# Kernel optimization log

Hardware: AMD Instinct MI355X
Metric: run time of the kernel (lower is better)

Reference implementation:

```python
import jax, jax.numpy as jnp
import numpy as np

B, N, C = 2, 2048, 256
L, H = 4, 4
HD = C // H  # 64, div=1 so q/k keep full head dim
EPS = 1e-5   # BatchNorm eps (eval mode, running_mean=0, running_var=1)


def setup_inputs() -> dict:
    key = jax.random.key(0)
    ks = jax.random.split(key, 20)
    w = lambda k, s: jax.random.normal(k, s, jnp.float32) * 0.05
    return {
        'x': jax.random.normal(ks[0], (B, N, C), jnp.float32),
        'in_w1': w(ks[1], (C, C)), 'in_b1': w(ks[2], (C,)),
        'in_g1': 1.0 + w(ks[3], (C,)), 'in_be1': w(ks[4], (C,)),
        'in_w2': w(ks[5], (C, C)), 'in_b2': w(ks[6], (C,)),
        'in_g2': 1.0 + w(ks[7], (C,)), 'in_be2': w(ks[8], (C,)),
        'q_w': w(ks[9], (L, H, HD, HD)), 'k_w': w(ks[10], (L, H, HD, HD)),
        'v_w': w(ks[11], (L, H, HD, HD)), 'v_b': w(ks[12], (L, H, HD)),
        't_w': w(ks[13], (L, H, HD, HD)), 't_b': w(ks[14], (L, H, HD)),
        'bn_g': 1.0 + w(ks[15], (L, H, HD)), 'bn_b': w(ks[16], (L, H, HD)),
        'proj_w': w(ks[17], (L, C, C)), 'proj_b': w(ks[18], (L, C)),
    }


def _bn(t, g, b):
    # eval-mode BatchNorm1d with running_mean=0, running_var=1
    return t * (g / jnp.sqrt(1.0 + EPS))[:, None] + b[:, None]


def _forward(x, in_w1, in_b1, in_g1, in_be1, in_w2, in_b2, in_g2, in_be2,
             q_w, k_w, v_w, v_b, t_w, t_b, bn_g, bn_b, proj_w, proj_b):
    Bq, Nq, Cq = x.shape
    h = x.transpose(0, 2, 1)  # (B, C, N)
    h = jax.nn.relu(_bn(jnp.einsum('oc,bcn->bon', in_w1, h) + in_b1[:, None], in_g1, in_be1))
    h = jax.nn.relu(_bn(jnp.einsum('oc,bcn->bon', in_w2, h) + in_b2[:, None], in_g2, in_be2))
    h = h.reshape(Bq, H, HD, Nq)  # split heads (B, H, hd, N)
    for l in range(L):
        xq = jnp.einsum('hoc,bhcn->bhno', q_w[l], h)                       # (B,H,N,hd)
        xk = jnp.einsum('hoc,bhcn->bhon', k_w[l], h)                       # (B,H,hd,N)
        xv = jnp.einsum('hoc,bhcn->bhon', v_w[l], h) + v_b[l][None, :, :, None]
        attn = jax.nn.softmax(jnp.einsum('bhno,bhom->bhnm', xq, xk), axis=-1)
        # offset-attention normalization: divide by column sums (torch dim=1)
        attn = attn / (1e-9 + attn.sum(axis=2, keepdims=True))
        xr = jnp.einsum('bhcn,bhnm->bhcm', xv, attn)                       # (B,H,hd,N)
        d = h - xr
        t = jnp.einsum('hoc,bhcn->bhon', t_w[l], d) + t_b[l][None, :, :, None]
        xr = jax.nn.relu(t * (bn_g[l] / jnp.sqrt(1.0 + EPS))[None, :, :, None]
                         + bn_b[l][None, :, :, None])
        h = h + xr
        hm = h.reshape(Bq, Cq, Nq)  # concat heads
        hm = jnp.einsum('oc,bcn->bon', proj_w[l], hm) + proj_b[l][:, None]
        h = hm.reshape(Bq, H, HD, Nq)
    return h.reshape(Bq, Cq, Nq).transpose(0, 2, 1)  # (B, N, C)


def reference(x, in_w1, in_b1, in_g1, in_be1, in_w2, in_b2, in_g2, in_be2,
              q_w, k_w, v_w, v_b, t_w, t_b, bn_g, bn_b, proj_w, proj_b):
    return _forward(x, in_w1, in_b1, in_g1, in_be1, in_w2, in_b2, in_g2, in_be2,
                    q_w, k_w, v_w, v_b, t_w, t_b, bn_g, bn_b, proj_w, proj_b)
```

## Files before the change

kernel.cpp:

```cpp
#include <hip/hip_runtime.h>
#include <math.h>

constexpr int NB = 2, NN = 2048, NC = 256, NL = 4, NH = 4, ND = 64;
constexpr float EPSV = 1e-5f;

using half8 = __attribute__((ext_vector_type(8))) _Float16;
using half4 = __attribute__((ext_vector_type(4))) _Float16;
using f32x4 = __attribute__((ext_vector_type(4))) float;

__device__ __forceinline__ f32x4 mfma16(half8 a, half8 b, f32x4 c) {
    return __builtin_amdgcn_mfma_f32_16x16x32_f16(a, b, c, 0, 0, 0);
}
__device__ __forceinline__ half8 cvt8(const float* p) {
    float4 x0 = *(const float4*)p, x1 = *(const float4*)(p + 4);
    half8 h;
    h[0]=(_Float16)x0.x; h[1]=(_Float16)x0.y; h[2]=(_Float16)x0.z; h[3]=(_Float16)x0.w;
    h[4]=(_Float16)x1.x; h[5]=(_Float16)x1.y; h[6]=(_Float16)x1.z; h[7]=(_Float16)x1.w;
    return h;
}

template<int EPI, bool INF16>
__global__ __launch_bounds__(256) void gemm_mfma(
    const float* __restrict__ Wg, const float* __restrict__ bias,
    const float* __restrict__ gam, const float* __restrict__ bet,
    const void* __restrict__ inp, _Float16* __restrict__ out16)
{
    int b = blockIdx.x, o0 = blockIdx.y * 64, n0 = blockIdx.z * 32;
    int t = threadIdx.x, w = t >> 6, li = t & 15, qd = (t >> 4) & 3;
    const float* wr = Wg + (size_t)(o0 + w * 16 + li) * NC + qd * 8;
    half8 af[8];
#pragma unroll
    for (int ks = 0; ks < 8; ++ks) af[ks] = cvt8(wr + ks * 32);
    f32x4 acc[2];
    acc[0] = {0.f, 0.f, 0.f, 0.f}; acc[1] = {0.f, 0.f, 0.f, 0.f};
#pragma unroll
    for (int ks = 0; ks < 8; ++ks) {
#pragma unroll
        for (int g = 0; g < 2; ++g) {
            int n = n0 + g * 16 + li;
            half8 bf;
            if (INF16) {
                bf = *(const half8*)((const _Float16*)inp +
                        ((size_t)(b * NN + n) * NC + ks * 32 + qd * 8));
            } else {
                bf = cvt8((const float*)inp + ((size_t)(b * NN + n) * NC + ks * 32 + qd * 8));
            }
            acc[g] = mfma16(af[ks], bf, acc[g]);
        }
    }
    int ob = o0 + w * 16 + qd * 4;
    float4 bs = *(const float4*)(bias + ob);
    float4 gs = {0,0,0,0}, be = {0,0,0,0};
    if (EPI == 1) { gs = *(const float4*)(gam + ob); be = *(const float4*)(bet + ob); }
    float scl = rsqrtf(1.f + EPSV);
#pragma unroll
    for (int g = 0; g < 2; ++g) {
        int n = n0 + g * 16 + li;
        half4 hv;
#pragma unroll
        for (int r = 0; r < 4; ++r) {
            float v = acc[g][r] + ((const float*)&bs)[r];
            if (EPI == 1)
                v = fmaxf(0.f, v * (((const float*)&gs)[r] * scl) + ((const float*)&be)[r]);
            hv[r] = (_Float16)v;
        }
        *(half4*)(out16 + (size_t)(b * NN + n) * NC + ob) = hv;
    }
}

__global__ __launch_bounds__(256) void qkv_fused(
    const float* __restrict__ qw, const float* __restrict__ kw,
    const float* __restrict__ vw, const float* __restrict__ vb,
    const _Float16* __restrict__ h16, _Float16* __restrict__ q16,
    _Float16* __restrict__ k16, _Float16* __restrict__ v16, int l)
{
    int bh = blockIdx.x, n0 = blockIdx.y * 64;
    int hh = bh & 3, b = bh >> 2;
    size_t wbase = (size_t)(l * NH + hh) * ND * ND;
    int t = threadIdx.x, w = t >> 6, li = t & 15, qd = (t >> 4) & 3;
    size_t wro = (size_t)(w * 16 + li) * ND + qd * 8;
    half8 aq0 = cvt8(qw + wbase + wro), aq1 = cvt8(qw + wbase + wro + 32);
    half8 ak0 = cvt8(kw + wbase + wro), ak1 = cvt8(kw + wbase + wro + 32);
    half8 av0 = cvt8(vw + wbase + wro), av1 = cvt8(vw + wbase + wro + 32);
    f32x4 accq[4], acck[4], accv[4];
#pragma unroll
    for (int g = 0; g < 4; ++g) {
        accq[g] = {0.f,0.f,0.f,0.f}; acck[g] = {0.f,0.f,0.f,0.f}; accv[g] = {0.f,0.f,0.f,0.f};
    }
#pragma unroll
    for (int g = 0; g < 4; ++g) {
        int n = n0 + g * 16 + li;
        const _Float16* hb = h16 + ((size_t)(b * NN + n) * NC + hh * 64 + qd * 8);
        half8 b0 = *(const half8*)(hb);
        half8 b1 = *(const half8*)(hb + 32);
        accq[g] = mfma16(aq0, b0, accq[g]); accq[g] = mfma16(aq1, b1, accq[g]);
        acck[g] = mfma16(ak0, b0, acck[g]); acck[g] = mfma16(ak1, b1, acck[g]);
        accv[g] = mfma16(av0, b0, accv[g]); accv[g] = mfma16(av1, b1, accv[g]);
    }
    int ob = w * 16 + qd * 4;
    _Float16* qo = q16 + (size_t)bh * NN * ND;
    _Float16* ko = k16 + (size_t)bh * NN * ND;
#pragma unroll
    for (int g = 0; g < 4; ++g) {
        int n = n0 + g * 16 + li;
        half4 hq, hk;
#pragma unroll
        for (int r = 0; r < 4; ++r) { hq[r] = (_Float16)accq[g][r]; hk[r] = (_Float16)acck[g][r]; }
        *(half4*)(qo + (size_t)n * ND + ob) = hq;
        *(half4*)(ko + (size_t)n * ND + ob) = hk;
    }
    float4 vb4 = *(const float4*)(vb + (size_t)(l * NH + hh) * ND + ob);
    _Float16* vo = v16 + (size_t)bh * ND * NN;
#pragma unroll
    for (int g = 0; g < 4; ++g) {
        int n = n0 + g * 16 + li;
#pragma unroll
        for (int r = 0; r < 4; ++r)
            vo[(size_t)(ob + r) * NN + n] = (_Float16)(accv[g][r] + ((const float*)&vb4)[r]);
    }
}

__global__ __launch_bounds__(256) void rowsum_part(
    const _Float16* __restrict__ qh, const _Float16* __restrict__ kh,
    float* __restrict__ rowsum_p)
{
    int bh = blockIdx.x, nt = blockIdx.y, ms = blockIdx.z;
    const _Float16* qp = qh + (size_t)bh * NN * ND;
    const _Float16* kp = kh + (size_t)bh * NN * ND;
    int t = threadIdx.x, w = t >> 6, li = t & 15, qd = (t >> 4) & 3;
    int nr = nt * 64 + w * 16;
    half8 aq0 = *(const half8*)(qp + (size_t)(nr + li) * ND + qd * 8);
    half8 aq1 = *(const half8*)(qp + (size_t)(nr + li) * ND + qd * 8 + 32);
    float rsacc[4] = {0.f, 0.f, 0.f, 0.f};
    for (int it = 0; it < 8; ++it) {
        int m0 = ms * 512 + it * 64;
        f32x4 s[4];
#pragma unroll
        for (int g = 0; g < 4; ++g) {
            const _Float16* kb = kp + (size_t)(m0 + g * 16 + li) * ND + qd * 8;
            half8 b0 = *(const half8*)(kb);
            half8 b1 = *(const half8*)(kb + 32);
            s[g] = {0.f, 0.f, 0.f, 0.f};
            s[g] = mfma16(aq0, b0, s[g]);
            s[g] = mfma16(aq1, b1, s[g]);
        }
#pragma unroll
        for (int r = 0; r < 4; ++r)
            rsacc[r] += __expf(s[0][r]) + __expf(s[1][r]) + __expf(s[2][r]) + __expf(s[3][r]);
    }
#pragma unroll
    for (int r = 0; r < 4; ++r) {
        float v = rsacc[r];
        v += __shfl_xor(v, 1); v += __shfl_xor(v, 2);
        v += __shfl_xor(v, 4); v += __shfl_xor(v, 8);
        if (li == 0) rowsum_p[((size_t)(ms * NB * NH + bh)) * NN + nr + qd * 4 + r] = v;
    }
}

__global__ __launch_bounds__(256) void attn_part(
    const _Float16* __restrict__ qh, const _Float16* __restrict__ kh,
    const _Float16* __restrict__ vh, const float* __restrict__ rowsum_p,
    _Float16* __restrict__ xrp16, float* __restrict__ csp)
{
    int bh = blockIdx.x, m0 = blockIdx.y * 64, ns = blockIdx.z;
    const _Float16* qp = qh + (size_t)bh * NN * ND;
    const _Float16* kp = kh + (size_t)bh * NN * ND;
    const _Float16* vp = vh + (size_t)bh * ND * NN;
    __shared__ __align__(16) _Float16 Plds[2][64 * 72];
    __shared__ float cs_wave[4][64];
    int t = threadIdx.x, w = t >> 6, li = t & 15, qd = (t >> 4) & 3;
    half8 bk[4][2];
#pragma unroll
    for (int g = 0; g < 4; ++g) {
        const _Float16* kb = kp + (size_t)(m0 + g * 16 + li) * ND + qd * 8;
        bk[g][0] = *(const half8*)(kb);
        bk[g][1] = *(const half8*)(kb + 32);
    }
    f32x4 acc[4];
#pragma unroll
    for (int g = 0; g < 4; ++g) acc[g] = {0.f, 0.f, 0.f, 0.f};
    float csacc[4] = {0.f, 0.f, 0.f, 0.f};
    for (int it = 0; it < 8; ++it) {
        int n0 = ns * 512 + it * 64;
        _Float16* Pb = Plds[it & 1];
        const _Float16* qrow = qp + (size_t)(n0 + w * 16 + li) * ND + qd * 8;
        half8 aq0 = *(const half8*)(qrow);
        half8 aq1 = *(const half8*)(qrow + 32);
        f32x4 s[4];
#pragma unroll
        for (int g = 0; g < 4; ++g) {
            s[g] = {0.f, 0.f, 0.f, 0.f};
            s[g] = mfma16(aq0, bk[g][0], s[g]);
            s[g] = mfma16(aq1, bk[g][1], s[g]);
        }
        int ridx = bh * NN + n0 + w * 16 + qd * 4;
        float4 r0 = *(const float4*)(rowsum_p + ridx);
        float4 r1 = *(const float4*)(rowsum_p + (size_t)NB * NH * NN + ridx);
        float4 r2 = *(const float4*)(rowsum_p + 2 * (size_t)NB * NH * NN + ridx);
        float4 r3 = *(const float4*)(rowsum_p + 3 * (size_t)NB * NH * NN + ridx);
        float irs[4];
        irs[0] = 1.f / (r0.x + r1.x + r2.x + r3.x);
        irs[1] = 1.f / (r0.y + r1.y + r2.y + r3.y);
        irs[2] = 1.f / (r0.z + r1.z + r2.z + r3.z);
        irs[3] = 1.f / (r0.w + r1.w + r2.w + r3.w);
#pragma unroll
        for (int g = 0; g < 4; ++g) {
            half4 pv; float lsum = 0.f;
#pragma unroll
            for (int r = 0; r < 4; ++r) {
                float p = __expf(s[g][r]) * irs[r];
                lsum += p;
                pv[r] = (_Float16)p;
            }
            csacc[g] += lsum;
            *(half4*)(&Pb[(g * 16 + li) * 72 + w * 16 + qd * 4]) = pv;
        }
        __syncthreads();
        const _Float16* vrow = vp + (size_t)(w * 16 + li) * NN + n0 + qd * 8;
        half8 av0 = *(const half8*)(vrow);
        half8 av1 = *(const half8*)(vrow + 32);
#pragma unroll
        for (int g = 0; g < 4; ++g) {
            half8 b0 = *(const half8*)(&Pb[(g * 16 + li) * 72 + qd * 8]);
            half8 b1 = *(const half8*)(&Pb[(g * 16 + li) * 72 + qd * 8 + 32]);
            acc[g] = mfma16(av0, b0, acc[g]);
            acc[g] = mfma16(av1, b1, acc[g]);
        }
    }
#pragma unroll
    for (int g = 0; g < 4; ++g) {
        float v = csacc[g];
        v += __shfl_xor(v, 16); v += __shfl_xor(v, 32);
        if (qd == 0) cs_wave[w][g * 16 + li] = v;
    }
    __syncthreads();
    if (t < 64) {
        float cs = cs_wave[0][t] + cs_wave[1][t] + cs_wave[2][t] + cs_wave[3][t];
        csp[((size_t)ns * NB * NH + bh) * NN + m0 + t] = cs;
    }
    _Float16* xo = xrp16 + (size_t)ns * ((size_t)NB * NC * NN);
#pragma unroll
    for (int g = 0; g < 4; ++g)
#pragma unroll
        for (int r = 0; r < 4; ++r)
            xo[(size_t)(bh * 64 + w * 16 + qd * 4 + r) * NN + m0 + g * 16 + li] =
                (_Float16)acc[g][r];
}

__global__ __launch_bounds__(256) void reduce_dx(
    const _Float16* __restrict__ xrp16, const float* __restrict__ csp,
    const _Float16* __restrict__ h16, _Float16* __restrict__ d16)
{
    int bh = blockIdx.x, n0 = blockIdx.y * 32, c0g = blockIdx.z * 32;
    int b = bh >> 2, cbase = (bh & 3) * 64 + c0g;
    __shared__ float ts[32][33];
    int t = threadIdx.x, xcol = t & 31, yr = t >> 5;
    int m = n0 + xcol;
    const size_t CSS = (size_t)NB * NH * NN;
    float cs = 1e-9f + csp[(size_t)bh * NN + m] + csp[CSS + bh * NN + m]
             + csp[2 * CSS + bh * NN + m] + csp[3 * CSS + bh * NN + m];
    float icv = 1.f / cs;
    const size_t XSS = (size_t)NB * NC * NN;
#pragma unroll
    for (int r = 0; r < 4; ++r) {
        int c = yr + 8 * r;
        size_t off = (size_t)(bh * 64 + c0g + c) * NN + m;
        float s = (float)xrp16[off] + (float)xrp16[XSS + off]
                + (float)xrp16[2 * XSS + off] + (float)xrp16[3 * XSS + off];
        ts[c][xcol] = s * icv;
    }
    __syncthreads();
#pragma unroll
    for (int r = 0; r < 4; ++r) {
        int n = n0 + yr + 8 * r;
        size_t off = (size_t)(b * NN + n) * NC + cbase + xcol;
        d16[off] = (_Float16)((float)h16[off] - ts[xcol][yr + 8 * r]);
    }
}

__global__ __launch_bounds__(256) void delta_mfma(
    const float* __restrict__ tw, const float* __restrict__ tb,
    const float* __restrict__ bng, const float* __restrict__ bnb,
    const _Float16* __restrict__ h16, const _Float16* __restrict__ d16,
    _Float16* __restrict__ hn16, int l)
{
    int bh = blockIdx.x, n0 = blockIdx.y * 32;
    int hh = bh & 3, b = bh >> 2;
    const float* wp = tw + (size_t)(l * NH + hh) * ND * ND;
    int t = threadIdx.x, w = t >> 6, li = t & 15, qd = (t >> 4) & 3;
    const float* wr = wp + (size_t)(w * 16 + li) * ND + qd * 8;
    half8 af0 = cvt8(wr), af1 = cvt8(wr + 32);
    f32x4 acc[2];
    acc[0] = {0.f, 0.f, 0.f, 0.f}; acc[1] = {0.f, 0.f, 0.f, 0.f};
#pragma unroll
    for (int g = 0; g < 2; ++g) {
        int n = n0 + g * 16 + li;
        const _Float16* db = d16 + ((size_t)(b * NN + n) * NC + hh * 64 + qd * 8);
        half8 b0 = *(const half8*)(db);
        half8 b1 = *(const half8*)(db + 32);
        acc[g] = mfma16(af0, b0, acc[g]);
        acc[g] = mfma16(af1, b1, acc[g]);
    }
    int ob = w * 16 + qd * 4;
    float4 tb4 = *(const float4*)(tb  + (size_t)(l * NH + hh) * ND + ob);
    float4 g4  = *(const float4*)(bng + (size_t)(l * NH + hh) * ND + ob);
    float4 b4  = *(const float4*)(bnb + (size_t)(l * NH + hh) * ND + ob);
    float scl = rsqrtf(1.f + EPSV);
#pragma unroll
    for (int g = 0; g < 2; ++g) {
        int n = n0 + g * 16 + li;
        size_t off = (size_t)(b * NN + n) * NC + hh * 64 + ob;
        half4 h4 = *(const half4*)(h16 + off);
        half4 hv;
#pragma unroll
        for (int r = 0; r < 4; ++r) {
            float tv = acc[g][r] + ((const float*)&tb4)[r];
            float x2 = fmaxf(0.f, tv * (((const float*)&g4)[r] * scl) + ((const float*)&b4)[r]);
            hv[r] = (_Float16)((float)h4[r] + x2);
        }
        *(half4*)(hn16 + off) = hv;
    }
}

__global__ __launch_bounds__(256) void final_out(
    const _Float16* __restrict__ h16, float* __restrict__ out)
{
    size_t e = ((size_t)blockIdx.x * 256 + threadIdx.x) * 4;
    half4 hv = *(const half4*)(h16 + e);
    float4 o;
    o.x = (float)hv[0]; o.y = (float)hv[1]; o.z = (float)hv[2]; o.w = (float)hv[3];
    *(float4*)(out + e) = o;
}

extern "C" void kernel_launch(void* const* d_in, const int* in_sizes, int n_in,
                              void* d_out, int out_size, void* d_ws, size_t ws_size,
                              hipStream_t stream)
{
    (void)in_sizes; (void)n_in; (void)out_size; (void)ws_size;
    const float* x      = (const float*)d_in[0];
    const float* in_w1  = (const float*)d_in[1];
    const float* in_b1  = (const float*)d_in[2];
    const float* in_g1  = (const float*)d_in[3];
    const float* in_be1 = (const float*)d_in[4];
    const float* in_w2  = (const float*)d_in[5];
    const float* in_b2  = (const float*)d_in[6];
    const float* in_g2  = (const float*)d_in[7];
    const float* in_be2 = (const float*)d_in[8];
    const float* q_w    = (const float*)d_in[9];
    const float* k_w    = (const float*)d_in[10];
    const float* v_w    = (const float*)d_in[11];
    const float* v_b    = (const float*)d_in[12];
    const float* t_w    = (const float*)d_in[13];
    const float* t_b    = (const float*)d_in[14];
    const float* bn_g   = (const float*)d_in[15];
    const float* bn_b   = (const float*)d_in[16];
    const float* proj_w = (const float*)d_in[17];
    const float* proj_b = (const float*)d_in[18];

    float* ws = (float*)d_ws;
    const size_t M = (size_t)NB * NC * NN;
    float* rowsum_p = ws;
    float* csp      = ws + 65536;
    _Float16* xrp16 = (_Float16*)(ws + 131072);
    _Float16* hbase = (_Float16*)(ws + 131072 + 2 * M);
    _Float16* h16  = hbase;
    _Float16* hA16 = hbase + M;
    _Float16* d16  = hbase + 2 * M;
    _Float16* q16  = hbase + 3 * M;
    _Float16* k16  = hbase + 4 * M;
    _Float16* v16  = hbase + 5 * M;

    dim3 g1(NB, NC / 64, NN / 32);

    gemm_mfma<1, false><<<g1, 256, 0, stream>>>(in_w1, in_b1, in_g1, in_be1, x,    hA16);
    gemm_mfma<1, true ><<<g1, 256, 0, stream>>>(in_w2, in_b2, in_g2, in_be2, hA16, h16);

    for (int l = 0; l < NL; l++) {
        qkv_fused<<<dim3(NB * NH, NN / 64), 256, 0, stream>>>(
            q_w, k_w, v_w, v_b, h16, q16, k16, v16, l);
        rowsum_part<<<dim3(NB * NH, NN / 64, 4), 256, 0, stream>>>(q16, k16, rowsum_p);
        attn_part<<<dim3(NB * NH, NN / 64, 4), 256, 0, stream>>>(
            q16, k16, v16, rowsum_p, xrp16, csp);
        reduce_dx<<<dim3(NB * NH, NN / 32, 2), 256, 0, stream>>>(xrp16, csp, h16, d16);
        delta_mfma<<<dim3(NB * NH, NN / 32), 256, 0, stream>>>(
            t_w, t_b, bn_g, bn_b, h16, d16, hA16, l);
        gemm_mfma<0, true><<<g1, 256, 0, stream>>>(proj_w + (size_t)l * NC * NC,
                                                   proj_b + (size_t)l * NC,
                                                   nullptr, nullptr, hA16, h16);
    }

    final_out<<<dim3(M / 1024), 256, 0, stream>>>(h16, (float*)d_out);
}
```

Baseline: 443.7 us.

## Fuse partial reduction into delta GEMM, raise attention split count, drop final cast

```diff
diff --git a/kernel.cpp b/kernel.cpp
--- a/kernel.cpp
+++ b/kernel.cpp
@@ -3,6 +3,7 @@
 
 constexpr int NB = 2, NN = 2048, NC = 256, NL = 4, NH = 4, ND = 64;
 constexpr float EPSV = 1e-5f;
+constexpr int NSPL = 8;
 
 using half8 = __attribute__((ext_vector_type(8))) _Float16;
 using half4 = __attribute__((ext_vector_type(4))) _Float16;
@@ -19,11 +20,11 @@
     return h;
 }
 
-template<int EPI, bool INF16>
+template<int EPI, bool INF16, bool OUT32>
 __global__ __launch_bounds__(256) void gemm_mfma(
     const float* __restrict__ Wg, const float* __restrict__ bias,
     const float* __restrict__ gam, const float* __restrict__ bet,
-    const void* __restrict__ inp, _Float16* __restrict__ out16)
+    const void* __restrict__ inp, void* __restrict__ outp)
 {
     int b = blockIdx.x, o0 = blockIdx.y * 64, n0 = blockIdx.z * 32;
     int t = threadIdx.x, w = t >> 6, li = t & 15, qd = (t >> 4) & 3;
@@ -56,15 +57,23 @@
 #pragma unroll
     for (int g = 0; g < 2; ++g) {
         int n = n0 + g * 16 + li;
-        half4 hv;
+        float v4[4];
 #pragma unroll
         for (int r = 0; r < 4; ++r) {
             float v = acc[g][r] + ((const float*)&bs)[r];
             if (EPI == 1)
                 v = fmaxf(0.f, v * (((const float*)&gs)[r] * scl) + ((const float*)&be)[r]);
-            hv[r] = (_Float16)v;
-        }
-        *(half4*)(out16 + (size_t)(b * NN + n) * NC + ob) = hv;
+            v4[r] = v;
+        }
+        if (OUT32) {
+            float4 fv = {v4[0], v4[1], v4[2], v4[3]};
+            *(float4*)((float*)outp + (size_t)(b * NN + n) * NC + ob) = fv;
+        } else {
+            half4 hv;
+#pragma unroll
+            for (int r = 0; r < 4; ++r) hv[r] = (_Float16)v4[r];
+            *(half4*)((_Float16*)outp + (size_t)(b * NN + n) * NC + ob) = hv;
+        }
     }
 }
 
@@ -74,7 +83,7 @@
     const _Float16* __restrict__ h16, _Float16* __restrict__ q16,
     _Float16* __restrict__ k16, _Float16* __restrict__ v16, int l)
 {
-    int bh = blockIdx.x, n0 = blockIdx.y * 64;
+    int bh = blockIdx.x, n0 = blockIdx.y * 32;
     int hh = bh & 3, b = bh >> 2;
     size_t wbase = (size_t)(l * NH + hh) * ND * ND;
     int t = threadIdx.x, w = t >> 6, li = t & 15, qd = (t >> 4) & 3;
@@ -82,13 +91,13 @@
     half8 aq0 = cvt8(qw + wbase + wro), aq1 = cvt8(qw + wbase + wro + 32);
     half8 ak0 = cvt8(kw + wbase + wro), ak1 = cvt8(kw + wbase + wro + 32);
     half8 av0 = cvt8(vw + wbase + wro), av1 = cvt8(vw + wbase + wro + 32);
-    f32x4 accq[4], acck[4], accv[4];
-#pragma unroll
-    for (int g = 0; g < 4; ++g) {
+    f32x4 accq[2], acck[2], accv[2];
+#pragma unroll
+    for (int g = 0; g < 2; ++g) {
         accq[g] = {0.f,0.f,0.f,0.f}; acck[g] = {0.f,0.f,0.f,0.f}; accv[g] = {0.f,0.f,0.f,0.f};
     }
 #pragma unroll
-    for (int g = 0; g < 4; ++g) {
+    for (int g = 0; g < 2; ++g) {
         int n = n0 + g * 16 + li;
         const _Float16* hb = h16 + ((size_t)(b * NN + n) * NC + hh * 64 + qd * 8);
         half8 b0 = *(const half8*)(hb);
@@ -101,7 +110,7 @@
     _Float16* qo = q16 + (size_t)bh * NN * ND;
     _Float16* ko = k16 + (size_t)bh * NN * ND;
 #pragma unroll
-    for (int g = 0; g < 4; ++g) {
+    for (int g = 0; g < 2; ++g) {
         int n = n0 + g * 16 + li;
         half4 hq, hk;
 #pragma unroll
@@ -112,7 +121,7 @@
     float4 vb4 = *(const float4*)(vb + (size_t)(l * NH + hh) * ND + ob);
     _Float16* vo = v16 + (size_t)bh * ND * NN;
 #pragma unroll
-    for (int g = 0; g < 4; ++g) {
+    for (int g = 0; g < 2; ++g) {
         int n = n0 + g * 16 + li;
 #pragma unroll
         for (int r = 0; r < 4; ++r)
@@ -132,8 +141,8 @@
     half8 aq0 = *(const half8*)(qp + (size_t)(nr + li) * ND + qd * 8);
     half8 aq1 = *(const half8*)(qp + (size_t)(nr + li) * ND + qd * 8 + 32);
     float rsacc[4] = {0.f, 0.f, 0.f, 0.f};
-    for (int it = 0; it < 8; ++it) {
-        int m0 = ms * 512 + it * 64;
+    for (int it = 0; it < NN / NSPL / 64; ++it) {
+        int m0 = ms * (NN / NSPL) + it * 64;
         f32x4 s[4];
 #pragma unroll
         for (int g = 0; g < 4; ++g) {
@@ -180,8 +189,9 @@
 #pragma unroll
     for (int g = 0; g < 4; ++g) acc[g] = {0.f, 0.f, 0.f, 0.f};
     float csacc[4] = {0.f, 0.f, 0.f, 0.f};
-    for (int it = 0; it < 8; ++it) {
-        int n0 = ns * 512 + it * 64;
+    const size_t RSS = (size_t)NB * NH * NN;
+    for (int it = 0; it < NN / NSPL / 64; ++it) {
+        int n0 = ns * (NN / NSPL) + it * 64;
         _Float16* Pb = Plds[it & 1];
         const _Float16* qrow = qp + (size_t)(n0 + w * 16 + li) * ND + qd * 8;
         half8 aq0 = *(const half8*)(qrow);
@@ -194,15 +204,13 @@
             s[g] = mfma16(aq1, bk[g][1], s[g]);
         }
         int ridx = bh * NN + n0 + w * 16 + qd * 4;
-        float4 r0 = *(const float4*)(rowsum_p + ridx);
-        float4 r1 = *(const float4*)(rowsum_p + (size_t)NB * NH * NN + ridx);
-        float4 r2 = *(const float4*)(rowsum_p + 2 * (size_t)NB * NH * NN + ridx);
-        float4 r3 = *(const float4*)(rowsum_p + 3 * (size_t)NB * NH * NN + ridx);
-        float irs[4];
-        irs[0] = 1.f / (r0.x + r1.x + r2.x + r3.x);
-        irs[1] = 1.f / (r0.y + r1.y + r2.y + r3.y);
-        irs[2] = 1.f / (r0.z + r1.z + r2.z + r3.z);
-        irs[3] = 1.f / (r0.w + r1.w + r2.w + r3.w);
+        float rs[4] = {0.f, 0.f, 0.f, 0.f};
+#pragma unroll
+        for (int sl = 0; sl < NSPL; ++sl) {
+            float4 rv = *(const float4*)(rowsum_p + sl * RSS + ridx);
+            rs[0] += rv.x; rs[1] += rv.y; rs[2] += rv.z; rs[3] += rv.w;
+        }
+        float irs[4] = {1.f / rs[0], 1.f / rs[1], 1.f / rs[2], 1.f / rs[3]};
 #pragma unroll
         for (int g = 0; g < 4; ++g) {
             half4 pv; float lsum = 0.f;
@@ -247,57 +255,54 @@
                 (_Float16)acc[g][r];
 }
 
-__global__ __launch_bounds__(256) void reduce_dx(
-    const _Float16* __restrict__ xrp16, const float* __restrict__ csp,
-    const _Float16* __restrict__ h16, _Float16* __restrict__ d16)
-{
-    int bh = blockIdx.x, n0 = blockIdx.y * 32, c0g = blockIdx.z * 32;
-    int b = bh >> 2, cbase = (bh & 3) * 64 + c0g;
-    __shared__ float ts[32][33];
-    int t = threadIdx.x, xcol = t & 31, yr = t >> 5;
-    int m = n0 + xcol;
-    const size_t CSS = (size_t)NB * NH * NN;
-    float cs = 1e-9f + csp[(size_t)bh * NN + m] + csp[CSS + bh * NN + m]
-             + csp[2 * CSS + bh * NN + m] + csp[3 * CSS + bh * NN + m];
-    float icv = 1.f / cs;
-    const size_t XSS = (size_t)NB * NC * NN;
-#pragma unroll
-    for (int r = 0; r < 4; ++r) {
-        int c = yr + 8 * r;
-        size_t off = (size_t)(bh * 64 + c0g + c) * NN + m;
-        float s = (float)xrp16[off] + (float)xrp16[XSS + off]
-                + (float)xrp16[2 * XSS + off] + (float)xrp16[3 * XSS + off];
-        ts[c][xcol] = s * icv;
-    }
-    __syncthreads();
-#pragma unroll
-    for (int r = 0; r < 4; ++r) {
-        int n = n0 + yr + 8 * r;
-        size_t off = (size_t)(b * NN + n) * NC + cbase + xcol;
-        d16[off] = (_Float16)((float)h16[off] - ts[xcol][yr + 8 * r]);
-    }
-}
-
-__global__ __launch_bounds__(256) void delta_mfma(
+__global__ __launch_bounds__(256) void delta_fused(
     const float* __restrict__ tw, const float* __restrict__ tb,
     const float* __restrict__ bng, const float* __restrict__ bnb,
-    const _Float16* __restrict__ h16, const _Float16* __restrict__ d16,
-    _Float16* __restrict__ hn16, int l)
+    const _Float16* __restrict__ xrp16, const float* __restrict__ csp,
+    const _Float16* __restrict__ h16, _Float16* __restrict__ hn16, int l)
 {
     int bh = blockIdx.x, n0 = blockIdx.y * 32;
     int hh = bh & 3, b = bh >> 2;
+    __shared__ float xt[64][33];
+    int t = threadIdx.x;
+    {
+        int xcol = t & 31, yr = t >> 5;
+        int m = n0 + xcol;
+        const size_t CSS = (size_t)NB * NH * NN;
+        float cs = 1e-9f;
+#pragma unroll
+        for (int sl = 0; sl < NSPL; ++sl) cs += csp[sl * CSS + (size_t)bh * NN + m];
+        float icv = 1.f / cs;
+        const size_t XSS = (size_t)NB * NC * NN;
+#pragma unroll
+        for (int r = 0; r < 8; ++r) {
+            int c = yr + 8 * r;
+            size_t off = (size_t)(bh * 64 + c) * NN + m;
+            float s = 0.f;
+#pragma unroll
+            for (int sl = 0; sl < NSPL; ++sl) s += (float)xrp16[sl * XSS + off];
+            xt[c][xcol] = s * icv;
+        }
+    }
+    __syncthreads();
+    int w = t >> 6, li = t & 15, qd = (t >> 4) & 3;
     const float* wp = tw + (size_t)(l * NH + hh) * ND * ND;
-    int t = threadIdx.x, w = t >> 6, li = t & 15, qd = (t >> 4) & 3;
     const float* wr = wp + (size_t)(w * 16 + li) * ND + qd * 8;
     half8 af0 = cvt8(wr), af1 = cvt8(wr + 32);
     f32x4 acc[2];
     acc[0] = {0.f, 0.f, 0.f, 0.f}; acc[1] = {0.f, 0.f, 0.f, 0.f};
 #pragma unroll
     for (int g = 0; g < 2; ++g) {
-        int n = n0 + g * 16 + li;
-        const _Float16* db = d16 + ((size_t)(b * NN + n) * NC + hh * 64 + qd * 8);
-        half8 b0 = *(const half8*)(db);
-        half8 b1 = *(const half8*)(db + 32);
+        int nl = g * 16 + li;
+        size_t hoff = (size_t)(b * NN + n0 + nl) * NC + hh * 64;
+        half8 h0 = *(const half8*)(h16 + hoff + qd * 8);
+        half8 h1 = *(const half8*)(h16 + hoff + 32 + qd * 8);
+        half8 b0, b1;
+#pragma unroll
+        for (int j = 0; j < 8; ++j) {
+            b0[j] = (_Float16)((float)h0[j] - xt[qd * 8 + j][nl]);
+            b1[j] = (_Float16)((float)h1[j] - xt[32 + qd * 8 + j][nl]);
+        }
         acc[g] = mfma16(af0, b0, acc[g]);
         acc[g] = mfma16(af1, b1, acc[g]);
     }
@@ -320,16 +325,6 @@
         }
         *(half4*)(hn16 + off) = hv;
     }
-}
-
-__global__ __launch_bounds__(256) void final_out(
-    const _Float16* __restrict__ h16, float* __restrict__ out)
-{
-    size_t e = ((size_t)blockIdx.x * 256 + threadIdx.x) * 4;
-    half4 hv = *(const half4*)(h16 + e);
-    float4 o;
-    o.x = (float)hv[0]; o.y = (float)hv[1]; o.z = (float)hv[2]; o.w = (float)hv[3];
-    *(float4*)(out + e) = o;
 }
 
 extern "C" void kernel_launch(void* const* d_in, const int* in_sizes, int n_in,
@@ -360,34 +355,36 @@
     float* ws = (float*)d_ws;
     const size_t M = (size_t)NB * NC * NN;
     float* rowsum_p = ws;
-    float* csp      = ws + 65536;
-    _Float16* xrp16 = (_Float16*)(ws + 131072);
-    _Float16* hbase = (_Float16*)(ws + 131072 + 2 * M);
+    float* csp      = ws + (size_t)NSPL * NB * NH * NN;
+    _Float16* xrp16 = (_Float16*)(csp + (size_t)NSPL * NB * NH * NN);
+    _Float16* hbase = (_Float16*)((float*)xrp16 + NSPL * M / 2);
     _Float16* h16  = hbase;
     _Float16* hA16 = hbase + M;
-    _Float16* d16  = hbase + 2 * M;
-    _Float16* q16  = hbase + 3 * M;
-    _Float16* k16  = hbase + 4 * M;
-    _Float16* v16  = hbase + 5 * M;
+    _Float16* q16  = hbase + 2 * M;
+    _Float16* k16  = hbase + 3 * M;
+    _Float16* v16  = hbase + 4 * M;
 
     dim3 g1(NB, NC / 64, NN / 32);
 
-    gemm_mfma<1, false><<<g1, 256, 0, stream>>>(in_w1, in_b1, in_g1, in_be1, x,    hA16);
-    gemm_mfma<1, true ><<<g1, 256, 0, stream>>>(in_w2, in_b2, in_g2, in_be2, hA16, h16);
+    gemm_mfma<1, false, false><<<g1, 256, 0, stream>>>(in_w1, in_b1, in_g1, in_be1, x,    hA16);
+    gemm_mfma<1, true,  false><<<g1, 256, 0, stream>>>(in_w2, in_b2, in_g2, in_be2, hA16, h16);
 
     for (int l = 0; l < NL; l++) {
-        qkv_fused<<<dim3(NB * NH, NN / 64), 256, 0, stream>>>(
+        qkv_fused<<<dim3(NB * NH, NN / 32), 256, 0, stream>>>(
             q_w, k_w, v_w, v_b, h16, q16, k16, v16, l);
-        rowsum_part<<<dim3(NB * NH, NN / 64, 4), 256, 0, stream>>>(q16, k16, rowsum_p);
-        attn_part<<<dim3(NB * NH, NN / 64, 4), 256, 0, stream>>>(
+        rowsum_part<<<dim3(NB * NH, NN / 64, NSPL), 256, 0, stream>>>(q16, k16, rowsum_p);
+        attn_part<<<dim3(NB * NH, NN / 64, NSPL), 256, 0, stream>>>(
             q16, k16, v16, rowsum_p, xrp16, csp);
-        reduce_dx<<<dim3(NB * NH, NN / 32, 2), 256, 0, stream>>>(xrp16, csp, h16, d16);
-        delta_mfma<<<dim3(NB * NH, NN / 32), 256, 0, stream>>>(
-            t_w, t_b, bn_g, bn_b, h16, d16, hA16, l);
-        gemm_mfma<0, true><<<g1, 256, 0, stream>>>(proj_w + (size_t)l * NC * NC,
-                                                   proj_b + (size_t)l * NC,
-                                                   nullptr, nullptr, hA16, h16);
-    }
-
-    final_out<<<dim3(M / 1024), 256, 0, stream>>>(h16, (float*)d_out);
-}
+        delta_fused<<<dim3(NB * NH, NN / 32), 256, 0, stream>>>(
+            t_w, t_b, bn_g, bn_b, xrp16, csp, h16, hA16, l);
+        if (l < NL - 1) {
+            gemm_mfma<0, true, false><<<g1, 256, 0, stream>>>(
+                proj_w + (size_t)l * NC * NC, proj_b + (size_t)l * NC,
+                nullptr, nullptr, hA16, h16);
+        } else {
+            gemm_mfma<0, true, true><<<g1, 256, 0, stream>>>(
+                proj_w + (size_t)l * NC * NC, proj_b + (size_t)l * NC,
+                nullptr, nullptr, hA16, d_out);
+        }
+    }
+}
```

Measured after the change: 506.7 us. 1.14x slower.
